# Kernel tuning notes

Hardware: AMD Instinct MI355X
Metric: run time of the kernel (lower is better)

## Reference

```python
import jax, jax.numpy as jnp
import numpy as np

H = 16  # n_heads (matches init_kwargs)


def setup_inputs() -> dict:
    key = jax.random.key(0)
    ks = jax.random.split(key, 11)
    B, L, D = 4, 2048, 1024
    inp = {
        "query": jax.random.normal(ks[0], (B, L, D), jnp.float32),
        "key": jax.random.normal(ks[1], (B, L, D), jnp.float32),
        "value": jax.random.normal(ks[2], (B, L, D), jnp.float32),
        "mask": jnp.ones((1, L, L), jnp.int32),
        "Wq": jax.random.normal(ks[3], (D, D), jnp.float32) / np.sqrt(D).astype(np.float32),
        "bq": jax.random.normal(ks[4], (D,), jnp.float32) * 0.02,
        "Wk": jax.random.normal(ks[5], (D, D), jnp.float32) / np.sqrt(D).astype(np.float32),
        "bk": jax.random.normal(ks[6], (D,), jnp.float32) * 0.02,
        "Wv": jax.random.normal(ks[7], (D, D), jnp.float32) / np.sqrt(D).astype(np.float32),
        "bv": jax.random.normal(ks[8], (D,), jnp.float32) * 0.02,
        "Wo": jax.random.normal(ks[9], (D, D), jnp.float32) / np.sqrt(D).astype(np.float32),
        "bo": jax.random.normal(ks[10], (D,), jnp.float32) * 0.02,
    }
    return inp


def reference(query, key, value, mask, Wq, bq, Wk, bk, Wv, bv, Wo, bo):
    B, L, D = query.shape
    dk = D // H
    scale = float(dk) ** -0.5

    def proj(x, W, b):
        # torch Linear: x @ W.T + b, then split heads -> (B, H, L, dk)
        return (x @ W.T + b).reshape(B, -1, H, dk).transpose(0, 2, 1, 3)

    q = proj(query, Wq, bq)
    k = proj(key, Wk, bk)
    v = proj(value, Wv, bv)

    scores = jnp.einsum('bhqd,bhkd->bhqk', q, k) * scale  # (B,H,L,L)
    # mask unsqueezed over head dim; masked_fill(mask == 0, -1e9)
    scores = jnp.where(mask[:, None, :, :] == 0, jnp.float32(-1e9), scores)
    p_attn = jax.nn.softmax(scores, axis=-1)  # dropout omitted (eval mode)
    x = jnp.einsum('bhqk,bhkd->bhqd', p_attn, v)
    x = x.transpose(0, 2, 1, 3).reshape(B, -1, D)
    return x @ Wo.T + bo
```

## Files before the change

kernel.cpp:

```cpp
#include <hip/hip_runtime.h>
#include <hip/hip_bf16.h>
#include <type_traits>


typedef __hip_bfloat16 bf16;
typedef __attribute__((ext_vector_type(8))) short s8;
typedef __attribute__((ext_vector_type(4))) short s4;
typedef __attribute__((ext_vector_type(4))) float f4;

constexpr int Bb = 4, Ls = 2048, Dd = 1024, Hh = 16, DK = 64;
constexpr int BHn = Bb * Hh;
constexpr int Mrows = Bb * Ls;

typedef const __attribute__((address_space(1))) unsigned int* gas_t;
typedef __attribute__((address_space(3))) unsigned int* las_t;
__device__ __forceinline__ void dma16(const void* g, void* l) {
    __builtin_amdgcn_global_load_lds((gas_t)g, (las_t)l, 16, 0, 0);
}

__device__ __forceinline__ s8 ld8(const float* __restrict__ p) {
    const float4 a = *(const float4*)p;
    const float4 b = *(const float4*)(p + 4);
    union { bf16 h[8]; s8 v; } u;
    u.h[0] = __float2bfloat16(a.x); u.h[1] = __float2bfloat16(a.y);
    u.h[2] = __float2bfloat16(a.z); u.h[3] = __float2bfloat16(a.w);
    u.h[4] = __float2bfloat16(b.x); u.h[5] = __float2bfloat16(b.y);
    u.h[6] = __float2bfloat16(b.z); u.h[7] = __float2bfloat16(b.w);
    return u.v;
}
__device__ __forceinline__ void st1(bf16* p, float v)  { *p = __float2bfloat16(v); }
__device__ __forceinline__ void st1(float* p, float v) { *p = v; }

__global__ __launch_bounds__(256) void conv_bf16(
    const float* __restrict__ in, bf16* __restrict__ out, int n8)
{
    const int i = blockIdx.x * 256 + threadIdx.x;
    if (i < n8) *(s8*)&out[(size_t)i * 8] = ld8(in + (size_t)i * 8);
}

template<int MODE, typename WT, typename OT>
__global__ __launch_bounds__(256) void gemm_nt(
    const bf16* __restrict__ A, const WT* __restrict__ W,
    const float* __restrict__ bias, OT* __restrict__ out,
    int M, int N, int K, float osc)
{
    __shared__ __align__(16) bf16 lA[128 * 32];
    __shared__ __align__(16) bf16 lB[128 * 32];
    const int tid  = threadIdx.x;
    const int wave = tid >> 6, lane = tid & 63;
    const int qd = lane >> 4, lr = lane & 15;
    const int wm = (wave & 1) * 64, wn = (wave >> 1) * 64;
    const int row0 = blockIdx.x * 128, col0 = blockIdx.y * 128;

    f4 acc[4][4] = {};

    const int c0 = tid, c1 = tid + 256;
    const int wr0 = c0 >> 2, wk0 = (c0 & 3) * 8;
    const int wr1 = c1 >> 2, wk1 = (c1 & 3) * 8;

    for (int kt = 0; kt < K; kt += 32) {
#pragma unroll
        for (int r = 0; r < 2; r++) {
            const int s = r * 256 + tid;
            const int row = s >> 2, c = s & 3;
            dma16(A + (size_t)(row0 + row) * K + kt + c * 8, &lA[s * 8]);
        }
        if constexpr (std::is_same<WT, bf16>::value) {
#pragma unroll
            for (int r = 0; r < 2; r++) {
                const int s = r * 256 + tid;
                const int row = s >> 2, c = s & 3;
                dma16(W + (size_t)(col0 + row) * K + kt + c * 8, &lB[s * 8]);
            }
        } else {
            *(s8*)&lB[c0 * 8] = ld8(W + (size_t)(col0 + wr0) * K + kt + wk0);
            *(s8*)&lB[c1 * 8] = ld8(W + (size_t)(col0 + wr1) * K + kt + wk1);
        }
        __syncthreads();
        s8 af[4], bfm[4];
#pragma unroll
        for (int i = 0; i < 4; i++) af[i]  = *(const s8*)&lA[(wm + i * 16 + lr) * 32 + qd * 8];
#pragma unroll
        for (int j = 0; j < 4; j++) bfm[j] = *(const s8*)&lB[(wn + j * 16 + lr) * 32 + qd * 8];
#pragma unroll
        for (int i = 0; i < 4; i++)
#pragma unroll
            for (int j = 0; j < 4; j++)
                acc[i][j] = __builtin_amdgcn_mfma_f32_16x16x32_bf16(af[i], bfm[j], acc[i][j], 0, 0, 0);
        __syncthreads();
    }

#pragma unroll
    for (int j = 0; j < 4; j++) {
        const int colg = col0 + wn + j * 16 + lr;
        const float bv = bias[colg];
#pragma unroll
        for (int i = 0; i < 4; i++) {
            const int rowb = row0 + wm + i * 16 + qd * 4;
            if (MODE == 2) {
                const int b = rowb >> 11, l = rowb & (Ls - 1);
                const int h = colg >> 6, d = colg & (DK - 1);
                union { bf16 h4[4]; s4 v; } u;
#pragma unroll
                for (int ri = 0; ri < 4; ri++)
                    u.h4[ri] = __float2bfloat16((acc[i][j][ri] + bv) * osc);
                *(s4*)&((bf16*)out)[(((size_t)(b * Hh + h) * DK) + d) * Ls + l] = u.v;
            } else {
#pragma unroll
                for (int ri = 0; ri < 4; ri++) {
                    const int rowg = rowb + ri;
                    const float v = (acc[i][j][ri] + bv) * osc;
                    size_t idx;
                    if (MODE == 0) {
                        idx = (size_t)rowg * N + colg;
                    } else {
                        const int b = rowg >> 11, l = rowg & (Ls - 1);
                        const int h = colg >> 6, d = colg & (DK - 1);
                        idx = (((size_t)(b * Hh + h) * Ls) + l) * DK + d;
                    }
                    st1(&out[idx], v);
                }
            }
        }
    }
}

__global__ __launch_bounds__(256) void pack_mask(
    const int* __restrict__ m, unsigned long long* __restrict__ bits)
{
    const int g = blockIdx.x * 256 + threadIdx.x;
    const unsigned long long b = __ballot(m[g] != 0);
    if ((threadIdx.x & 63) == 0) bits[g >> 6] = b;
}

__global__ __launch_bounds__(512, 2) void attn(
    const bf16* __restrict__ Q, const bf16* __restrict__ K,
    const bf16* __restrict__ Vt, const unsigned long long* __restrict__ mbits,
    bf16* __restrict__ X)
{
    __shared__ __align__(16) bf16 lK[2][64 * 64];
    __shared__ __align__(16) bf16 lV[2][64 * 64];

    const int blk = blockIdx.x;
    const int bh = blk >> 4;
    const int q0 = (blk & 15) * 128;
    const int tid = threadIdx.x;
    const int wave = tid >> 6, lane = tid & 63;
    const int qd = lane >> 4, lr = lane & 15;
    const int qw0 = q0 + wave * 16;

    const bf16* Qb = Q  + (size_t)bh * Ls * DK;
    const bf16* Kb = K  + (size_t)bh * Ls * DK;
    const bf16* Vb = Vt + (size_t)bh * DK * Ls;

    const s8 bq0 = *(const s8*)(Qb + (size_t)(qw0 + lr) * DK + qd * 8);
    const s8 bq1 = *(const s8*)(Qb + (size_t)(qw0 + lr) * DK + 32 + qd * 8);

    f4 o[4] = {};
    float lp = 0.f;

    const int srcA = ((lane & 16) << 1) + lr;
    const bool hiSel = (lane & 32) != 0;

    const int srow = tid >> 3, scs = tid & 7;
    const int sc = scs ^ (srow & 7);
    const bf16* gK = Kb + (size_t)srow * DK + sc * 8;
    const bf16* gV = Vb + (size_t)srow * Ls + sc * 8;

    const size_t mrow = (size_t)(qw0 + lr) * (Ls / 64);

    dma16(gK, &lK[0][tid * 8]);
    dma16(gV, &lV[0][tid * 8]);
    unsigned long long wcur = mbits[mrow];
    asm volatile("s_waitcnt vmcnt(0)" ::: "memory");
    __builtin_amdgcn_s_barrier();

    int cur = 0;
    for (int kt = 0; kt < Ls / 64; ++kt) {
        unsigned long long wnext = 0;
        if (kt + 1 < Ls / 64) {
            const int nb = cur ^ 1;
            dma16(gK + (size_t)(kt + 1) * 64 * DK, &lK[nb][tid * 8]);
            dma16(gV + (size_t)(kt + 1) * 64,      &lV[nb][tid * 8]);
            wnext = mbits[mrow + kt + 1];
        }

        f4 st[4];
        __builtin_amdgcn_s_setprio(1);
#pragma unroll
        for (int mt = 0; mt < 4; mt++) {
            const int rowk = mt * 16 + lr;
            const s8 ak0 = *(const s8*)&lK[cur][(rowk * 8 + ((qd)     ^ (rowk & 7))) * 8];
            const s8 ak1 = *(const s8*)&lK[cur][(rowk * 8 + ((4 + qd) ^ (rowk & 7))) * 8];
            f4 z = {};
            z = __builtin_amdgcn_mfma_f32_16x16x32_bf16(ak0, bq0, z, 0, 0, 0);
            z = __builtin_amdgcn_mfma_f32_16x16x32_bf16(ak1, bq1, z, 0, 0, 0);
            st[mt] = z;
        }
        __builtin_amdgcn_s_setprio(0);

        if (__ballot(wcur == ~0ULL) != ~0ULL) {
#pragma unroll
            for (int mt = 0; mt < 4; mt++)
#pragma unroll
                for (int ri = 0; ri < 4; ri++) {
                    const int kbit = mt * 16 + qd * 4 + ri;
                    if (!((wcur >> kbit) & 1ULL)) st[mt][ri] = -1e9f;
                }
        }

        unsigned pk[4][2];
#pragma unroll
        for (int mt = 0; mt < 4; mt++) {
#pragma unroll
            for (int u = 0; u < 2; u++) {
                const float p0 = __builtin_amdgcn_exp2f(st[mt][2 * u]);
                const float p1 = __builtin_amdgcn_exp2f(st[mt][2 * u + 1]);
                lp += p0 + p1;
                unsigned r;
                asm("v_cvt_pk_bf16_f32 %0, %1, %2" : "=v"(r) : "v"(p0), "v"(p1));
                pk[mt][u] = r;
            }
        }

#pragma unroll
        for (int h = 0; h < 2; h++) {
            const unsigned f0a = __shfl((int)pk[2 * h][0],     srcA, 64);
            const unsigned f0b = __shfl((int)pk[2 * h + 1][0], srcA, 64);
            const unsigned f1a = __shfl((int)pk[2 * h][1],     srcA, 64);
            const unsigned f1b = __shfl((int)pk[2 * h + 1][1], srcA, 64);
            const unsigned f2a = __shfl((int)pk[2 * h][0],     srcA + 16, 64);
            const unsigned f2b = __shfl((int)pk[2 * h + 1][0], srcA + 16, 64);
            const unsigned f3a = __shfl((int)pk[2 * h][1],     srcA + 16, 64);
            const unsigned f3b = __shfl((int)pk[2 * h + 1][1], srcA + 16, 64);
            union { unsigned u[4]; s8 v; } bp;
            bp.u[0] = hiSel ? f0b : f0a;
            bp.u[1] = hiSel ? f1b : f1a;
            bp.u[2] = hiSel ? f2b : f2a;
            bp.u[3] = hiSel ? f3b : f3a;
            __builtin_amdgcn_s_setprio(1);
#pragma unroll
            for (int dt = 0; dt < 4; dt++) {
                const int rowd = dt * 16 + lr;
                const s8 av = *(const s8*)&lV[cur][(rowd * 8 + ((h * 4 + qd) ^ (rowd & 7))) * 8];
                o[dt] = __builtin_amdgcn_mfma_f32_16x16x32_bf16(av, bp.v, o[dt], 0, 0, 0);
            }
            __builtin_amdgcn_s_setprio(0);
        }

        asm volatile("s_waitcnt vmcnt(0) lgkmcnt(0)" ::: "memory");
        __builtin_amdgcn_s_barrier();
        cur ^= 1;
        wcur = wnext;
    }

    float lsum = lp;
    lsum += __shfl_xor(lsum, 16, 64);
    lsum += __shfl_xor(lsum, 32, 64);
    const int b = bh >> 4, head = bh & 15;
    const float inv = 1.f / lsum;
    const int qrow = qw0 + lr;
#pragma unroll
    for (int dt = 0; dt < 4; dt++) {
        union { bf16 h4[4]; s4 v; } u;
#pragma unroll
        for (int ri = 0; ri < 4; ri++)
            u.h4[ri] = __float2bfloat16(o[dt][ri] * inv);
        *(s4*)&X[((size_t)(b * Ls + qrow)) * Dd + head * 64 + dt * 16 + qd * 4] = u.v;
    }
}

extern "C" void kernel_launch(void* const* d_in, const int* in_sizes, int n_in,
                              void* d_out, int out_size, void* d_ws, size_t ws_size,
                              hipStream_t stream) {
    const float* q_in = (const float*)d_in[0];
    const float* k_in = (const float*)d_in[1];
    const float* v_in = (const float*)d_in[2];
    const int*   mask = (const int*)d_in[3];
    const float* Wq = (const float*)d_in[4];  const float* bq = (const float*)d_in[5];
    const float* Wk = (const float*)d_in[6];  const float* bk = (const float*)d_in[7];
    const float* Wv = (const float*)d_in[8];  const float* bv = (const float*)d_in[9];
    const float* Wo = (const float*)d_in[10]; const float* bo = (const float*)d_in[11];
    float* out = (float*)d_out;

    char* ws = (char*)d_ws;
    const size_t sz = (size_t)BHn * Ls * DK * sizeof(bf16);
    bf16* S0 = (bf16*)(ws);
    bf16* S1 = (bf16*)(ws + sz);
    bf16* S2 = (bf16*)(ws + 2 * sz);
    bf16* S3 = (bf16*)(ws + 3 * sz);
    unsigned long long* mb = (unsigned long long*)(ws + 4 * sz);
    const int NW = Dd * Dd;

    dim3 gg(Mrows / 128, Dd / 128);
    const int gA = (Mrows * Dd / 8 + 255) / 256;
    const int gW = (NW / 8 + 255) / 256;

    const float QSC = 0.125f * 1.44269504f;

    conv_bf16<<<gA, 256, 0, stream>>>(v_in, S0, Mrows * Dd / 8);
    conv_bf16<<<gW, 256, 0, stream>>>(Wv, S1, NW / 8);
    gemm_nt<2, bf16, bf16><<<gg, 256, 0, stream>>>(S0, S1, bv, S3, Mrows, Dd, Dd, 1.0f);

    conv_bf16<<<gA, 256, 0, stream>>>(k_in, S0, Mrows * Dd / 8);
    conv_bf16<<<gW, 256, 0, stream>>>(Wk, S1 + NW, NW / 8);
    gemm_nt<1, bf16, bf16><<<gg, 256, 0, stream>>>(S0, S1 + NW, bk, S2, Mrows, Dd, Dd, 1.0f);

    conv_bf16<<<gA, 256, 0, stream>>>(q_in, S0, Mrows * Dd / 8);
    gemm_nt<1, float, bf16><<<gg, 256, 0, stream>>>(S0, Wq, bq, S1, Mrows, Dd, Dd, QSC);

    pack_mask<<<(Ls * Ls) / 256, 256, 0, stream>>>(mask, mb);
    attn<<<BHn * (Ls / 128), 512, 0, stream>>>(S1, S2, S3, mb, S0);

    conv_bf16<<<gW, 256, 0, stream>>>(Wo, S2, NW / 8);
    gemm_nt<0, bf16, float><<<gg, 256, 0, stream>>>(S0, S2, bo, out, Mrows, Dd, Dd, 1.0f);
}
```

Measured before the change: 446.6 us.

## Permute K tile rows to drop P-fragment shuffles and use single-buffered LDS

The attention kernel now reads K rows from LDS in a permuted order, with a matching mask-bit mapping and a new XOR swizzle. The QK^T accumulator layout then lines up with the B-operand layout of the PV MFMA, so the eight cross-lane shuffles and selects per half-tile go away. Separately, the double-buffered K/V LDS tiles are replaced by a single buffer: each tile is loaded, the block synchronizes, computes, then synchronizes again. This halves LDS use and simplifies the loop, but it gives up overlapping the next tile's DMA with compute and relies on other resident waves to hide load latency.

Result: faster. 416.3 us (-6.8%).

```diff
diff --git a/kernel.cpp b/kernel.cpp
--- a/kernel.cpp
+++ b/kernel.cpp
@@ -138,8 +138,8 @@
     const bf16* __restrict__ Vt, const unsigned long long* __restrict__ mbits,
     bf16* __restrict__ X)
 {
-    __shared__ __align__(16) bf16 lK[2][64 * 64];
-    __shared__ __align__(16) bf16 lV[2][64 * 64];
+    __shared__ __align__(16) bf16 lK[64 * 64];
+    __shared__ __align__(16) bf16 lV[64 * 64];
 
     const int blk = blockIdx.x;
     const int bh = blk >> 4;
@@ -159,39 +159,27 @@
     f4 o[4] = {};
     float lp = 0.f;
 
-    const int srcA = ((lane & 16) << 1) + lr;
-    const bool hiSel = (lane & 32) != 0;
-
     const int srow = tid >> 3, scs = tid & 7;
-    const int sc = scs ^ (srow & 7);
+    const int sc = scs ^ ((srow & 3) | ((srow >> 1) & 4));
     const bf16* gK = Kb + (size_t)srow * DK + sc * 8;
     const bf16* gV = Vb + (size_t)srow * Ls + sc * 8;
 
     const size_t mrow = (size_t)(qw0 + lr) * (Ls / 64);
 
-    dma16(gK, &lK[0][tid * 8]);
-    dma16(gV, &lV[0][tid * 8]);
-    unsigned long long wcur = mbits[mrow];
-    asm volatile("s_waitcnt vmcnt(0)" ::: "memory");
-    __builtin_amdgcn_s_barrier();
-
-    int cur = 0;
     for (int kt = 0; kt < Ls / 64; ++kt) {
-        unsigned long long wnext = 0;
-        if (kt + 1 < Ls / 64) {
-            const int nb = cur ^ 1;
-            dma16(gK + (size_t)(kt + 1) * 64 * DK, &lK[nb][tid * 8]);
-            dma16(gV + (size_t)(kt + 1) * 64,      &lV[nb][tid * 8]);
-            wnext = mbits[mrow + kt + 1];
-        }
+        dma16(gK + (size_t)kt * 64 * DK, &lK[tid * 8]);
+        dma16(gV + (size_t)kt * 64,      &lV[tid * 8]);
+        const unsigned long long wcur = mbits[mrow + kt];
+        __syncthreads();
 
         f4 st[4];
         __builtin_amdgcn_s_setprio(1);
 #pragma unroll
         for (int mt = 0; mt < 4; mt++) {
-            const int rowk = mt * 16 + lr;
-            const s8 ak0 = *(const s8*)&lK[cur][(rowk * 8 + ((qd)     ^ (rowk & 7))) * 8];
-            const s8 ak1 = *(const s8*)&lK[cur][(rowk * 8 + ((4 + qd) ^ (rowk & 7))) * 8];
+            const int rk = 32 * (mt >> 1) + 8 * (lr >> 2) + 4 * (mt & 1) + (lr & 3);
+            const int fr = (rk & 3) | ((rk >> 1) & 4);
+            const s8 ak0 = *(const s8*)&lK[(rk * 8 + ((qd)     ^ fr)) * 8];
+            const s8 ak1 = *(const s8*)&lK[(rk * 8 + ((4 + qd) ^ fr)) * 8];
             f4 z = {};
             z = __builtin_amdgcn_mfma_f32_16x16x32_bf16(ak0, bq0, z, 0, 0, 0);
             z = __builtin_amdgcn_mfma_f32_16x16x32_bf16(ak1, bq1, z, 0, 0, 0);
@@ -204,7 +192,7 @@
             for (int mt = 0; mt < 4; mt++)
 #pragma unroll
                 for (int ri = 0; ri < 4; ri++) {
-                    const int kbit = mt * 16 + qd * 4 + ri;
+                    const int kbit = 32 * (mt >> 1) + 8 * qd + 4 * (mt & 1) + ri;
                     if (!((wcur >> kbit) & 1ULL)) st[mt][ri] = -1e9f;
                 }
         }
@@ -225,33 +213,23 @@
 
 #pragma unroll
         for (int h = 0; h < 2; h++) {
-            const unsigned f0a = __shfl((int)pk[2 * h][0],     srcA, 64);
-            const unsigned f0b = __shfl((int)pk[2 * h + 1][0], srcA, 64);
-            const unsigned f1a = __shfl((int)pk[2 * h][1],     srcA, 64);
-            const unsigned f1b = __shfl((int)pk[2 * h + 1][1], srcA, 64);
-            const unsigned f2a = __shfl((int)pk[2 * h][0],     srcA + 16, 64);
-            const unsigned f2b = __shfl((int)pk[2 * h + 1][0], srcA + 16, 64);
-            const unsigned f3a = __shfl((int)pk[2 * h][1],     srcA + 16, 64);
-            const unsigned f3b = __shfl((int)pk[2 * h + 1][1], srcA + 16, 64);
             union { unsigned u[4]; s8 v; } bp;
-            bp.u[0] = hiSel ? f0b : f0a;
-            bp.u[1] = hiSel ? f1b : f1a;
-            bp.u[2] = hiSel ? f2b : f2a;
-            bp.u[3] = hiSel ? f3b : f3a;
+            bp.u[0] = pk[2 * h][0];
+            bp.u[1] = pk[2 * h][1];
+            bp.u[2] = pk[2 * h + 1][0];
+            bp.u[3] = pk[2 * h + 1][1];
             __builtin_amdgcn_s_setprio(1);
 #pragma unroll
             for (int dt = 0; dt < 4; dt++) {
                 const int rowd = dt * 16 + lr;
-                const s8 av = *(const s8*)&lV[cur][(rowd * 8 + ((h * 4 + qd) ^ (rowd & 7))) * 8];
+                const int fv = (rowd & 3) | ((rowd >> 1) & 4);
+                const s8 av = *(const s8*)&lV[(rowd * 8 + ((h * 4 + qd) ^ fv)) * 8];
                 o[dt] = __builtin_amdgcn_mfma_f32_16x16x32_bf16(av, bp.v, o[dt], 0, 0, 0);
             }
             __builtin_amdgcn_s_setprio(0);
         }
 
-        asm volatile("s_waitcnt vmcnt(0) lgkmcnt(0)" ::: "memory");
-        __builtin_amdgcn_s_barrier();
-        cur ^= 1;
-        wcur = wnext;
+        __syncthreads();
     }
 
     float lsum = lp;
```
